# Performance work log

Hardware: AMD Instinct MI355X
Metric: run time of the kernel (lower is better)

The kernel has to match this reference:

```python
import math
import jax, jax.numpy as jnp
import numpy as np

B, T, D = 8, 2048, 512


def setup_inputs() -> dict:
    key = jax.random.key(0)
    kx, = jax.random.split(key, 1)
    x = jax.random.normal(kx, (B, T, D), dtype=jnp.float32)
    log_tau = jnp.asarray(math.log(2.0), dtype=jnp.float32)
    log_blend = jnp.asarray(math.log(0.3 / 0.7), dtype=jnp.float32)
    return {"x": x, "log_tau": log_tau, "log_blend": log_blend}


def _gelu_tanh(x):
    c = math.sqrt(2.0 / math.pi)
    return 0.5 * x * (1.0 + jnp.tanh(c * (x + 0.044715 * x * x * x)))


def reference(x, log_tau, log_blend):
    Bb, Tt, Dd = x.shape
    tau = jnp.exp(log_tau)
    alpha = jax.nn.sigmoid(log_blend)
    # F.normalize(x, dim=-1): divide by L2 norm clamped to eps=1e-12
    norm = jnp.maximum(jnp.linalg.norm(x, axis=-1, keepdims=True), 1e-12)
    x_norm = x / norm
    # cosine self-similarity [B, T, T]
    sim = jnp.einsum("btd,bsd->bts", x_norm, x_norm)
    # triu(diagonal=0) masks j >= i (current + future positions)
    causal_mask = jnp.triu(jnp.ones((Tt, Tt), dtype=bool), k=0)
    sim_causal = jnp.where(causal_mask[None, :, :], -jnp.inf, sim)
    max_sim = jnp.max(sim_causal, axis=-1)  # [B, T]; row 0 is -inf
    max_sim = jnp.nan_to_num(max_sim, nan=0.0, posinf=1.0, neginf=-1.0)
    novelty = jnp.exp(-tau * max_sim)
    scale = (1.0 - alpha + alpha * novelty)[..., None]  # [B, T, 1]
    return _gelu_tanh(x * scale)
```

## Files before the change

kernel.cpp:

```cpp
#include <hip/hip_runtime.h>

#define B_ 8
#define T_ 2048
#define D_ 512
#define BT 128
#define BK 64
#define NT (T_/BT)
#define NTILES (NT*(NT+1)/2)

typedef float f32x4 __attribute__((ext_vector_type(4)));
typedef __bf16 bf16x8 __attribute__((ext_vector_type(8)));

__device__ __forceinline__ unsigned encf(float f) {
    int i = __float_as_int(f);
    return (i < 0) ? ~((unsigned)i) : (((unsigned)i) | 0x80000000u);
}
__device__ __forceinline__ float decf(unsigned u) {
    unsigned b = (u & 0x80000000u) ? (u ^ 0x80000000u) : ~u;
    return __int_as_float((int)b);
}

__device__ __forceinline__ void gload_lds16(const __bf16* g, __bf16* l) {
    __builtin_amdgcn_global_load_lds(
        (const __attribute__((address_space(1))) unsigned int*)g,
        (__attribute__((address_space(3))) unsigned int*)l, 16, 0, 0);
}

__global__ __launch_bounds__(256) void rownorm_kernel(
        const float* __restrict__ x, __bf16* __restrict__ xn,
        unsigned* __restrict__ msim) {
    int row  = blockIdx.x * 4 + (threadIdx.x >> 6);
    int lane = threadIdx.x & 63;
    const float* p = x + (size_t)row * D_ + lane * 8;
    float4 a = *(const float4*)p;
    float4 b = *(const float4*)(p + 4);
    float ss = a.x*a.x + a.y*a.y + a.z*a.z + a.w*a.w
             + b.x*b.x + b.y*b.y + b.z*b.z + b.w*b.w;
#pragma unroll
    for (int m = 32; m; m >>= 1) ss += __shfl_xor(ss, m);
    float r = 1.0f / fmaxf(sqrtf(ss), 1e-12f);
    bf16x8 h;
    h[0] = (__bf16)(a.x * r); h[1] = (__bf16)(a.y * r);
    h[2] = (__bf16)(a.z * r); h[3] = (__bf16)(a.w * r);
    h[4] = (__bf16)(b.x * r); h[5] = (__bf16)(b.y * r);
    h[6] = (__bf16)(b.z * r); h[7] = (__bf16)(b.w * r);
    *(bf16x8*)(xn + (size_t)row * D_ + lane * 8) = h;
    if (lane == 0) msim[row] = 0x407FFFFFu;
}

__global__ __launch_bounds__(256, 2) void simmax_kernel(
        const __bf16* __restrict__ xn, unsigned* __restrict__ msim) {
    __shared__ __attribute__((aligned(16))) __bf16 sA[2][BT * BK];
    __shared__ __attribute__((aligned(16))) __bf16 sB[2][BT * BK];

    int bid = blockIdx.x;
    int b   = bid & 7;
    int s   = bid >> 3;
    int it  = 0;
    while ((it + 1) * (it + 2) / 2 <= s) it++;
    int jt  = s - it * (it + 1) / 2;
    const bool diag = (it == jt);

    int tid  = threadIdx.x;
    int lane = tid & 63;
    int w    = tid >> 6;
    int wr   = w >> 1;
    int wc   = w & 1;
    int fr   = lane & 15;
    int kg   = lane >> 4;

    const size_t rowA0 = (size_t)b * T_ + (size_t)it * BT;
    const size_t rowB0 = (size_t)b * T_ + (size_t)jt * BT;

    int rb   = lane >> 3;
    int csrc = (lane & 7) ^ rb;
    const __bf16* gA0 = xn + (rowA0 + w * 32 + rb) * D_ + csrc * 8;
    const __bf16* gB0 = xn + (rowB0 + w * 32 + rb) * D_ + csrc * 8;

    f32x4 acc[4][4];
#pragma unroll
    for (int m = 0; m < 4; m++)
#pragma unroll
        for (int n = 0; n < 4; n++)
            acc[m][n] = (f32x4){0.f, 0.f, 0.f, 0.f};

    int swz = (fr & 7) << 4;
    int laA = (wr * 64 + fr) * 128 + kg * 16;
    int laB = (wc * 64 + fr) * 128 + kg * 16;

    auto stage = [&](int buf, int kc) {
        int k0 = kc * BK;
#pragma unroll
        for (int p = 0; p < 4; p++) {
            gload_lds16(gA0 + (size_t)p * 8 * D_ + k0,
                        &sA[buf][(w * 32 + p * 8) * BK]);
            if (!diag)
                gload_lds16(gB0 + (size_t)p * 8 * D_ + k0,
                            &sB[buf][(w * 32 + p * 8) * BK]);
        }
    };

    auto compute = [&](int buf) {
        const char* bA = (const char*)&sA[buf][0];
        const char* bB = diag ? (const char*)&sA[buf][0]
                              : (const char*)&sB[buf][0];
#pragma unroll
        for (int ks = 0; ks < 2; ks++) {
            bf16x8 af[4], bfr[4];
#pragma unroll
            for (int n = 0; n < 4; n++)
                bfr[n] = *(const bf16x8*)(bB +
                           ((laB + n * 2048 + ks * 64) ^ swz));
#pragma unroll
            for (int m = 0; m < 4; m++)
                af[m] = *(const bf16x8*)(bA +
                           ((laA + m * 2048 + ks * 64) ^ swz));
#pragma unroll
            for (int m = 0; m < 4; m++)
#pragma unroll
                for (int n = 0; n < 4; n++)
                    acc[m][n] = __builtin_amdgcn_mfma_f32_16x16x32_bf16(
                        af[m], bfr[n], acc[m][n], 0, 0, 0);
        }
    };

    stage(0, 0);
    __syncthreads();
    for (int kc = 0; kc < D_ / BK; kc++) {
        int cur = kc & 1;
        if (kc < D_ / BK - 1) stage(cur ^ 1, kc + 1);
        compute(cur);
        __syncthreads();
    }

    unsigned* mrow = msim + (size_t)b * T_ + (size_t)it * BT;
    const float NINF = -__builtin_inff();
#pragma unroll
    for (int m = 0; m < 4; m++) {
#pragma unroll
        for (int e = 0; e < 4; e++) {
            int rloc = wr * 64 + m * 16 + kg * 4 + e;
            float v = NINF;
#pragma unroll
            for (int n = 0; n < 4; n++) {
                int cloc = wc * 64 + n * 16 + fr;
                float t = acc[m][n][e];
                if (diag && cloc >= rloc) t = NINF;
                v = fmaxf(v, t);
            }
            v = fmaxf(v, __shfl_xor(v, 1));
            v = fmaxf(v, __shfl_xor(v, 2));
            v = fmaxf(v, __shfl_xor(v, 4));
            v = fmaxf(v, __shfl_xor(v, 8));
            if (fr == 0) atomicMax(&mrow[rloc], encf(v));
        }
    }
}

__global__ __launch_bounds__(256) void gelu_kernel(
        const float* __restrict__ x, const unsigned* __restrict__ msim,
        const float* __restrict__ ltau, const float* __restrict__ lblend,
        float* __restrict__ out) {
    int i = blockIdx.x * 256 + threadIdx.x;
    float tau   = __expf(ltau[0]);
    float alpha = 1.f / (1.f + __expf(-lblend[0]));
    int row = i >> 7;
    float ms = decf(msim[row]);
    float sc = (1.f - alpha) + alpha * __expf(-tau * ms);
    float4 v = ((const float4*)x)[i];
    const float c0 = 0.7978845608028654f;
    const float c1 = 0.044715f;
    float4 o;
#pragma unroll
    for (int j = 0; j < 4; j++) {
        float z = ((const float*)&v)[j] * sc;
        float u = c0 * (z + c1 * z * z * z);
        float t = __expf(2.f * u);
        float th = 1.f - 2.f / (t + 1.f);
        ((float*)&o)[j] = 0.5f * z * (1.f + th);
    }
    ((float4*)out)[i] = o;
}

extern "C" void kernel_launch(void* const* d_in, const int* in_sizes, int n_in,
                              void* d_out, int out_size, void* d_ws, size_t ws_size,
                              hipStream_t stream) {
    (void)in_sizes; (void)n_in; (void)out_size; (void)ws_size;
    const float* x      = (const float*)d_in[0];
    const float* ltau   = (const float*)d_in[1];
    const float* lblend = (const float*)d_in[2];
    float*    out   = (float*)d_out;
    __bf16*   xn    = (__bf16*)d_out;
    unsigned* msim  = (unsigned*)d_ws;

    rownorm_kernel<<<B_ * T_ / 4, 256, 0, stream>>>(x, xn, msim);
    simmax_kernel<<<B_ * NTILES, 256, 0, stream>>>(xn, msim);
    gelu_kernel<<<(B_ * T_ * D_ / 4) / 256, 256, 0, stream>>>(x, msim, ltau, lblend, out);
}
```

Measured before the change: 63.15 us.

## Restructure simmax K-loop into split-phase pipeline with manual waitcnt and one barrier

```diff
diff --git a/kernel.cpp b/kernel.cpp
--- a/kernel.cpp
+++ b/kernel.cpp
@@ -7,6 +7,7 @@
 #define BK 64
 #define NT (T_/BT)
 #define NTILES (NT*(NT+1)/2)
+#define KTILES (D_/BK)
 
 typedef float f32x4 __attribute__((ext_vector_type(4)));
 typedef __bf16 bf16x8 __attribute__((ext_vector_type(8)));
@@ -74,8 +75,8 @@
 
     int rb   = lane >> 3;
     int csrc = (lane & 7) ^ rb;
-    const __bf16* gA0 = xn + (rowA0 + w * 32 + rb) * D_ + csrc * 8;
-    const __bf16* gB0 = xn + (rowB0 + w * 32 + rb) * D_ + csrc * 8;
+    const __bf16* gA = xn + (rowA0 + w * 8 + rb) * D_ + csrc * 8;
+    const __bf16* gB = xn + (rowB0 + w * 8 + rb) * D_ + csrc * 8;
 
     f32x4 acc[4][4];
 #pragma unroll
@@ -88,50 +89,90 @@
     int laA = (wr * 64 + fr) * 128 + kg * 16;
     int laB = (wc * 64 + fr) * 128 + kg * 16;
 
-    auto stage = [&](int buf, int kc) {
-        int k0 = kc * BK;
-#pragma unroll
-        for (int p = 0; p < 4; p++) {
-            gload_lds16(gA0 + (size_t)p * 8 * D_ + k0,
-                        &sA[buf][(w * 32 + p * 8) * BK]);
-            if (!diag)
-                gload_lds16(gB0 + (size_t)p * 8 * D_ + k0,
-                            &sB[buf][(w * 32 + p * 8) * BK]);
+#define STAGE_A(buf, kc) do {                                              \
+    _Pragma("unroll")                                                      \
+    for (int p = 0; p < 4; p++)                                            \
+        gload_lds16(gA + (size_t)p * 32 * D_ + (kc) * BK,                  \
+                    &sA[buf][(p * 32 + w * 8) * BK]);                      \
+} while (0)
+#define STAGE_B(buf, kc) do {                                              \
+    _Pragma("unroll")                                                      \
+    for (int p = 0; p < 4; p++)                                            \
+        gload_lds16(gB + (size_t)p * 32 * D_ + (kc) * BK,                  \
+                    &sB[buf][(p * 32 + w * 8) * BK]);                      \
+} while (0)
+
+    STAGE_A(0, 0);
+    if (!diag) STAGE_B(0, 0);
+
+    for (int kc = 0; kc < KTILES; kc++) {
+        int cur = kc & 1, nxt = cur ^ 1;
+        if (kc < KTILES - 1) {
+            STAGE_A(nxt, kc + 1);
+            asm volatile("s_waitcnt vmcnt(4)" ::: "memory");
+        } else {
+            asm volatile("s_waitcnt vmcnt(0)" ::: "memory");
         }
-    };
-
-    auto compute = [&](int buf) {
-        const char* bA = (const char*)&sA[buf][0];
-        const char* bB = diag ? (const char*)&sA[buf][0]
-                              : (const char*)&sB[buf][0];
-#pragma unroll
-        for (int ks = 0; ks < 2; ks++) {
-            bf16x8 af[4], bfr[4];
-#pragma unroll
-            for (int n = 0; n < 4; n++)
-                bfr[n] = *(const bf16x8*)(bB +
-                           ((laB + n * 2048 + ks * 64) ^ swz));
-#pragma unroll
-            for (int m = 0; m < 4; m++)
-                af[m] = *(const bf16x8*)(bA +
-                           ((laA + m * 2048 + ks * 64) ^ swz));
-#pragma unroll
-            for (int m = 0; m < 4; m++)
-#pragma unroll
-                for (int n = 0; n < 4; n++)
+        __builtin_amdgcn_sched_barrier(0);
+        asm volatile("s_barrier" ::: "memory");
+        __builtin_amdgcn_sched_barrier(0);
+
+        const char* bA = (const char*)&sA[cur][0];
+        const char* bB = diag ? (const char*)&sA[cur][0]
+                              : (const char*)&sB[cur][0];
+
+        bf16x8 af[4][2], b0[2][2];
+#pragma unroll
+        for (int m = 0; m < 4; m++)
+#pragma unroll
+            for (int ks = 0; ks < 2; ks++)
+                af[m][ks] = *(const bf16x8*)(bA +
+                              ((laA + m * 2048 + ks * 64) ^ swz));
+#pragma unroll
+        for (int n = 0; n < 2; n++)
+#pragma unroll
+            for (int ks = 0; ks < 2; ks++)
+                b0[n][ks] = *(const bf16x8*)(bB +
+                              ((laB + n * 2048 + ks * 64) ^ swz));
+        asm volatile("s_waitcnt lgkmcnt(0)" ::: "memory");
+        __builtin_amdgcn_sched_barrier(0);
+        __builtin_amdgcn_s_setprio(1);
+#pragma unroll
+        for (int m = 0; m < 4; m++)
+#pragma unroll
+            for (int n = 0; n < 2; n++)
+#pragma unroll
+                for (int ks = 0; ks < 2; ks++)
                     acc[m][n] = __builtin_amdgcn_mfma_f32_16x16x32_bf16(
-                        af[m], bfr[n], acc[m][n], 0, 0, 0);
-        }
-    };
-
-    stage(0, 0);
-    __syncthreads();
-    for (int kc = 0; kc < D_ / BK; kc++) {
-        int cur = kc & 1;
-        if (kc < D_ / BK - 1) stage(cur ^ 1, kc + 1);
-        compute(cur);
-        __syncthreads();
+                        af[m][ks], b0[n][ks], acc[m][n], 0, 0, 0);
+        __builtin_amdgcn_s_setprio(0);
+        __builtin_amdgcn_sched_barrier(0);
+
+        if (kc < KTILES - 1 && !diag) STAGE_B(nxt, kc + 1);
+
+        bf16x8 b1[2][2];
+#pragma unroll
+        for (int n = 0; n < 2; n++)
+#pragma unroll
+            for (int ks = 0; ks < 2; ks++)
+                b1[n][ks] = *(const bf16x8*)(bB +
+                              ((laB + (n + 2) * 2048 + ks * 64) ^ swz));
+        asm volatile("s_waitcnt lgkmcnt(0)" ::: "memory");
+        __builtin_amdgcn_sched_barrier(0);
+        __builtin_amdgcn_s_setprio(1);
+#pragma unroll
+        for (int m = 0; m < 4; m++)
+#pragma unroll
+            for (int n = 0; n < 2; n++)
+#pragma unroll
+                for (int ks = 0; ks < 2; ks++)
+                    acc[m][n + 2] = __builtin_amdgcn_mfma_f32_16x16x32_bf16(
+                        af[m][ks], b1[n][ks], acc[m][n + 2], 0, 0, 0);
+        __builtin_amdgcn_s_setprio(0);
+        __builtin_amdgcn_sched_barrier(0);
     }
+#undef STAGE_A
+#undef STAGE_B
 
     unsigned* mrow = msim + (size_t)b * T_ + (size_t)it * BT;
     const float NINF = -__builtin_inff();
```

Measured after the change: 63.35 us. Within noise of the previous version (+0.3%).
